# Kernel optimization log

Measured on AMD Instinct MI355X. Metric: run time of the kernel, lower is better.

The kernel has to match this reference:

```python
import jax, jax.numpy as jnp
import numpy as np

IN_FEATURES = 4096
OUT_FEATURES = 11008
N_TOKENS = 8192


def setup_inputs() -> dict:
    key = jax.random.key(0)
    kx, kw, kb = jax.random.split(key, 3)
    x = jax.random.normal(kx, (N_TOKENS, IN_FEATURES), dtype=jnp.float32)
    # nn.Linear weight: [out_features, in_features]
    bound = 1.0 / np.sqrt(IN_FEATURES)
    weight = jax.random.uniform(kw, (OUT_FEATURES, IN_FEATURES), dtype=jnp.float32,
                                minval=-bound, maxval=bound)
    bias = jax.random.uniform(kb, (OUT_FEATURES,), dtype=jnp.float32,
                              minval=-bound, maxval=bound)
    return {"x": x, "weight": weight, "bias": bias}


def reference(x, weight, bias):
    # Ternarize weights to {-1, 0, +1} then standard dense matmul + bias.
    ternary_w = jnp.sign(weight)  # [out, in]
    return jnp.matmul(x, ternary_w.T) + bias  # [n_tokens, out]
```

## Files before the change

kernel.cpp:

```cpp
#include <hip/hip_runtime.h>
#include <stdint.h>

#define M_DIM 8192
#define N_DIM 11008
#define K_DIM 4096

#define BM 256
#define BN 256
#define BK 64
#define NT (K_DIM / BK)
#define GRID_M (M_DIM / BM)
#define GRID_N (N_DIM / BN)
#define NWG (GRID_M * GRID_N)

#define BUF (BM * BK)
#define NRING 4

typedef int i32x4 __attribute__((ext_vector_type(4)));

__device__ __forceinline__ void gload16(const int8_t* src, int8_t* dst) {
    __builtin_amdgcn_global_load_lds(
        (const __attribute__((address_space(1))) uint32_t*)src,
        (__attribute__((address_space(3))) uint32_t*)dst, 16, 0, 0);
}


__global__ __launch_bounds__(256) void prepass_kernel(
    const float* __restrict__ x, int8_t* __restrict__ xq, float* __restrict__ sinv,
    const float* __restrict__ w, int8_t* __restrict__ wq, long long n16)
{
    if (blockIdx.x < 2048) {
        const int wave = blockIdx.x * 4 + (threadIdx.x >> 6);
        const int lane = threadIdx.x & 63;
        const float* row = x + (size_t)wave * K_DIM;

        float4 v[16];
        float mx = 0.0f;
        #pragma unroll
        for (int j = 0; j < 16; ++j) {
            v[j] = *(const float4*)(row + (j * 64 + lane) * 4);
            mx = fmaxf(mx, fmaxf(fmaxf(fabsf(v[j].x), fabsf(v[j].y)),
                                 fmaxf(fabsf(v[j].z), fabsf(v[j].w))));
        }
        #pragma unroll
        for (int off = 32; off > 0; off >>= 1)
            mx = fmaxf(mx, __shfl_xor(mx, off));
        if (mx < 1e-30f) mx = 1e-30f;
        const float s = 127.0f / mx;

        int8_t* orow = xq + (size_t)wave * K_DIM;
        #pragma unroll
        for (int j = 0; j < 16; ++j) {
            int a = (int)__builtin_rintf(v[j].x * s);
            int b = (int)__builtin_rintf(v[j].y * s);
            int c = (int)__builtin_rintf(v[j].z * s);
            int d = (int)__builtin_rintf(v[j].w * s);
            uint32_t p = (uint32_t)(a & 0xFF) | ((uint32_t)(b & 0xFF) << 8) |
                         ((uint32_t)(c & 0xFF) << 16) | ((uint32_t)(d & 0xFF) << 24);
            *(uint32_t*)(orow + (j * 64 + lane) * 4) = p;
        }
        if (lane == 0) sinv[wave] = mx / 127.0f;
    } else {
        long long i = (long long)(blockIdx.x - 2048) * blockDim.x + threadIdx.x;
        const long long stride = 2048LL * blockDim.x;
        for (; i < n16; i += stride) {
            const float* src = w + i * 16;
            uint32_t pk[4];
            #pragma unroll
            for (int q = 0; q < 4; ++q) {
                float4 f = *(const float4*)(src + q * 4);
                int a = (f.x > 0.f) ? 1 : ((f.x < 0.f) ? -1 : 0);
                int b = (f.y > 0.f) ? 1 : ((f.y < 0.f) ? -1 : 0);
                int c = (f.z > 0.f) ? 1 : ((f.z < 0.f) ? -1 : 0);
                int d = (f.w > 0.f) ? 1 : ((f.w < 0.f) ? -1 : 0);
                pk[q] = (uint32_t)(a & 0xFF) | ((uint32_t)(b & 0xFF) << 8) |
                        ((uint32_t)(c & 0xFF) << 16) | ((uint32_t)(d & 0xFF) << 24);
            }
            *(i32x4*)(wq + i * 16) = (i32x4){(int)pk[0], (int)pk[1], (int)pk[2], (int)pk[3]};
        }
    }
}


__global__ __launch_bounds__(1024, 4) void ternary_gemm_i8(
    const int8_t* __restrict__ A, const int8_t* __restrict__ B,
    const float* __restrict__ bias, const float* __restrict__ sinv,
    float* __restrict__ out)
{
    extern __shared__ int8_t lds[];
    int8_t* As = lds;
    int8_t* Bs = lds + NRING * BUF;

    const int tid  = threadIdx.x;
    const int lane = tid & 63;
    const int wid  = tid >> 6;
    const int wr   = wid >> 2;
    const int wc   = wid & 3;
    const int l15  = lane & 15;
    const int l4   = lane >> 4;

    const int bid = blockIdx.x;
    const int swz = (bid & 7) * (NWG / 8) + (bid >> 3);
    const int bm  = swz / GRID_N;
    const int bn  = swz % GRID_N;
    const long brow = (long)bm * BM;
    const long bcol = (long)bn * BN;

    const int rowt = tid >> 2;
    const int ssrc = (tid & 3) ^ ((tid >> 3) & 3);
    const int8_t* pA = A + (size_t)(brow + rowt) * K_DIM + ssrc * 16;
    const int8_t* pB = B + (size_t)(bcol + rowt) * K_DIM + ssrc * 16;

    auto stageAB = [&](int t, int bslot) {
        gload16(pA + (size_t)t * BK, As + bslot * BUF + tid * 16);
        gload16(pB + (size_t)t * BK, Bs + bslot * BUF + tid * 16);
    };

    const int slot = l4 ^ ((l15 >> 1) & 3);
    const int aOff = (wr * 64 + l15) * 64 + slot * 16;
    const int bOff = (wc * 64 + l15) * 64 + slot * 16;

    i32x4 acc[4][4];
    #pragma unroll
    for (int m = 0; m < 4; ++m)
        #pragma unroll
        for (int n = 0; n < 4; ++n) acc[m][n] = (i32x4){0, 0, 0, 0};

    stageAB(0, 0); stageAB(1, 1); stageAB(2, 2);
    asm volatile("s_waitcnt vmcnt(4)" ::: "memory");
    __builtin_amdgcn_s_barrier();
    __builtin_amdgcn_sched_barrier(0);

    for (int t = 0; t < NT; ++t) {
        const int b = t & 3;

        i32x4 ar[4], br[4];
        #pragma unroll
        for (int n = 0; n < 4; ++n)
            br[n] = *(const i32x4*)(Bs + b * BUF + n * 1024 + bOff);
        #pragma unroll
        for (int m = 0; m < 4; ++m)
            ar[m] = *(const i32x4*)(As + b * BUF + m * 1024 + aOff);

        if (t + 3 < NT) stageAB(t + 3, (t + 3) & 3);

        __builtin_amdgcn_s_setprio(1);
        #pragma unroll
        for (int m = 0; m < 4; ++m)
            #pragma unroll
            for (int n = 0; n < 4; ++n)
                acc[m][n] = __builtin_amdgcn_mfma_i32_16x16x64_i8(ar[m], br[n], acc[m][n], 0, 0, 0);
        __builtin_amdgcn_s_setprio(0);
        __builtin_amdgcn_sched_barrier(0);

        if (t <= NT - 4)      { asm volatile("s_waitcnt vmcnt(4)" ::: "memory"); }
        else if (t == NT - 3) { asm volatile("s_waitcnt vmcnt(2)" ::: "memory"); }
        else                  { asm volatile("s_waitcnt vmcnt(0)" ::: "memory"); }
        __builtin_amdgcn_s_barrier();
        __builtin_amdgcn_sched_barrier(0);
    }

    int   cols[4];
    float bv[4];
    #pragma unroll
    for (int n = 0; n < 4; ++n) {
        cols[n] = (int)bcol + wc * 64 + n * 16 + l15;
        bv[n] = bias[cols[n]];
    }
    #pragma unroll
    for (int m = 0; m < 4; ++m) {
        const size_t row0 = (size_t)brow + wr * 64 + m * 16 + l4 * 4;
        float s0 = sinv[row0], s1 = sinv[row0 + 1], s2 = sinv[row0 + 2], s3 = sinv[row0 + 3];
        #pragma unroll
        for (int n = 0; n < 4; ++n) {
            out[(row0 + 0) * N_DIM + cols[n]] = (float)acc[m][n][0] * s0 + bv[n];
            out[(row0 + 1) * N_DIM + cols[n]] = (float)acc[m][n][1] * s1 + bv[n];
            out[(row0 + 2) * N_DIM + cols[n]] = (float)acc[m][n][2] * s2 + bv[n];
            out[(row0 + 3) * N_DIM + cols[n]] = (float)acc[m][n][3] * s3 + bv[n];
        }
    }
}


__global__ void naive_kernel(const float* __restrict__ x, const float* __restrict__ w,
                             const float* __restrict__ bias, float* __restrict__ out) {
    long long o = (long long)blockIdx.x * blockDim.x + threadIdx.x;
    if (o >= (long long)M_DIM * N_DIM) return;
    int row = (int)(o / N_DIM), col = (int)(o % N_DIM);
    float s = 0.0f;
    const float* xr = x + (size_t)row * K_DIM;
    const float* wr = w + (size_t)col * K_DIM;
    for (int k = 0; k < K_DIM; ++k) {
        float wv = wr[k];
        s += (wv > 0.0f) ? xr[k] : ((wv < 0.0f) ? -xr[k] : 0.0f);
    }
    out[o] = s + bias[col];
}


extern "C" void kernel_launch(void* const* d_in, const int* in_sizes, int n_in,
                              void* d_out, int out_size, void* d_ws, size_t ws_size,
                              hipStream_t stream) {
    const float* x    = (const float*)d_in[0];
    const float* w    = (const float*)d_in[1];
    const float* bias = (const float*)d_in[2];
    float* out        = (float*)d_out;

    const size_t xq_bytes = (size_t)M_DIM * K_DIM;
    const size_t wq_bytes = (size_t)N_DIM * K_DIM;
    const size_t si_bytes = (size_t)M_DIM * sizeof(float);

    if (ws_size >= xq_bytes + wq_bytes + si_bytes) {
        int8_t* xq   = (int8_t*)d_ws;
        int8_t* wq   = (int8_t*)((char*)d_ws + xq_bytes);
        float*  sinv = (float*)((char*)d_ws + xq_bytes + wq_bytes);

        const long long n16 = ((long long)N_DIM * K_DIM) / 16;
        prepass_kernel<<<4096, 256, 0, stream>>>(x, xq, sinv, w, wq, n16);

        const int lds_bytes = NRING * 2 * BUF;
        hipFuncSetAttribute(reinterpret_cast<const void*>(ternary_gemm_i8),
                            hipFuncAttributeMaxDynamicSharedMemorySize, lds_bytes);
        ternary_gemm_i8<<<NWG, 1024, lds_bytes, stream>>>(xq, wq, bias, sinv, out);
    } else {
        const long long total = (long long)M_DIM * N_DIM;
        naive_kernel<<<(int)((total + 255) / 256), 256, 0, stream>>>(x, w, bias, out);
    }
}
```

Baseline: 462.0 us.

## Pre-swizzle ternary weights into MFMA fragment layout and load B directly to registers

The weight prepass now writes the int8 ternary weights in a layout that matches each wave's MFMA B-fragment order, so the GEMM loads B fragments straight from global memory into registers instead of staging them through LDS. This halves LDS usage and LDS traffic per tile, and the block ordering changes to iterate M fastest within the swizzle. The tradeoff is that B loads are no longer shared across the four waves in a row via LDS, so each B byte is fetched from global/L2 by four waves, and those direct loads sit on the critical path with no prefetch distance.

```diff
diff --git a/kernel.cpp b/kernel.cpp
--- a/kernel.cpp
+++ b/kernel.cpp
@@ -13,7 +13,7 @@
 #define GRID_N (N_DIM / BN)
 #define NWG (GRID_M * GRID_N)
 
-#define BUF (BM * BK)
+#define BUFA 16384
 #define NRING 4
 
 typedef int i32x4 __attribute__((ext_vector_type(4)));
@@ -27,7 +27,7 @@
 
 __global__ __launch_bounds__(256) void prepass_kernel(
     const float* __restrict__ x, int8_t* __restrict__ xq, float* __restrict__ sinv,
-    const float* __restrict__ w, int8_t* __restrict__ wq, long long n16)
+    const float* __restrict__ w, int8_t* __restrict__ wq)
 {
     if (blockIdx.x < 2048) {
         const int wave = blockIdx.x * 4 + (threadIdx.x >> 6);
@@ -61,10 +61,19 @@
         }
         if (lane == 0) sinv[wave] = mx / 127.0f;
     } else {
-        long long i = (long long)(blockIdx.x - 2048) * blockDim.x + threadIdx.x;
+        const long long total = 44032LL * 64;
+        long long gi = (long long)(blockIdx.x - 2048) * blockDim.x + threadIdx.x;
         const long long stride = 2048LL * blockDim.x;
-        for (; i < n16; i += stride) {
-            const float* src = w + i * 16;
+        for (; gi < total; gi += stride) {
+            const int lane  = (int)(gi & 63);
+            const long long chunk = gi >> 6;
+            const int t  = (int)(chunk & 63);
+            const int n  = (int)((chunk >> 6) & 3);
+            const int wc = (int)((chunk >> 8) & 3);
+            const int bn = (int)(chunk >> 10);
+            const int col = bn * 256 + wc * 64 + n * 16 + (lane & 15);
+            const int kb  = t * 64 + (lane >> 4) * 16;
+            const float* src = w + (size_t)col * K_DIM + kb;
             uint32_t pk[4];
             #pragma unroll
             for (int q = 0; q < 4; ++q) {
@@ -76,20 +85,20 @@
                 pk[q] = (uint32_t)(a & 0xFF) | ((uint32_t)(b & 0xFF) << 8) |
                         ((uint32_t)(c & 0xFF) << 16) | ((uint32_t)(d & 0xFF) << 24);
             }
-            *(i32x4*)(wq + i * 16) = (i32x4){(int)pk[0], (int)pk[1], (int)pk[2], (int)pk[3]};
+            *(i32x4*)(wq + chunk * 1024 + lane * 16) =
+                (i32x4){(int)pk[0], (int)pk[1], (int)pk[2], (int)pk[3]};
         }
     }
 }
 
 
 __global__ __launch_bounds__(1024, 4) void ternary_gemm_i8(
-    const int8_t* __restrict__ A, const int8_t* __restrict__ B,
+    const int8_t* __restrict__ A, const int8_t* __restrict__ Bq,
     const float* __restrict__ bias, const float* __restrict__ sinv,
     float* __restrict__ out)
 {
     extern __shared__ int8_t lds[];
     int8_t* As = lds;
-    int8_t* Bs = lds + NRING * BUF;
 
     const int tid  = threadIdx.x;
     const int lane = tid & 63;
@@ -101,24 +110,26 @@
 
     const int bid = blockIdx.x;
     const int swz = (bid & 7) * (NWG / 8) + (bid >> 3);
-    const int bm  = swz / GRID_N;
-    const int bn  = swz % GRID_N;
+    const int bm  = swz % GRID_M;
+    const int bn  = swz / GRID_M;
     const long brow = (long)bm * BM;
     const long bcol = (long)bn * BN;
 
     const int rowt = tid >> 2;
     const int ssrc = (tid & 3) ^ ((tid >> 3) & 3);
     const int8_t* pA = A + (size_t)(brow + rowt) * K_DIM + ssrc * 16;
-    const int8_t* pB = B + (size_t)(bcol + rowt) * K_DIM + ssrc * 16;
-
-    auto stageAB = [&](int t, int bslot) {
-        gload16(pA + (size_t)t * BK, As + bslot * BUF + tid * 16);
-        gload16(pB + (size_t)t * BK, Bs + bslot * BUF + tid * 16);
+
+    auto stageA = [&](int t, int bslot) {
+        gload16(pA + (size_t)t * BK, As + bslot * BUFA + tid * 16);
     };
 
     const int slot = l4 ^ ((l15 >> 1) & 3);
     const int aOff = (wr * 64 + l15) * 64 + slot * 16;
-    const int bOff = (wc * 64 + l15) * 64 + slot * 16;
+
+    const int8_t* pBn[4];
+    #pragma unroll
+    for (int n = 0; n < 4; ++n)
+        pBn[n] = Bq + ((((size_t)bn * 4 + wc) * 4 + n) * 64) * 1024 + (size_t)lane * 16;
 
     i32x4 acc[4][4];
     #pragma unroll
@@ -126,23 +137,25 @@
         #pragma unroll
         for (int n = 0; n < 4; ++n) acc[m][n] = (i32x4){0, 0, 0, 0};
 
-    stageAB(0, 0); stageAB(1, 1); stageAB(2, 2);
-    asm volatile("s_waitcnt vmcnt(4)" ::: "memory");
+    stageA(0, 0); stageA(1, 1); stageA(2, 2);
+    asm volatile("s_waitcnt vmcnt(2)" ::: "memory");
     __builtin_amdgcn_s_barrier();
     __builtin_amdgcn_sched_barrier(0);
 
     for (int t = 0; t < NT; ++t) {
         const int b = t & 3;
 
-        i32x4 ar[4], br[4];
+        i32x4 br[4];
         #pragma unroll
         for (int n = 0; n < 4; ++n)
-            br[n] = *(const i32x4*)(Bs + b * BUF + n * 1024 + bOff);
+            br[n] = *(const i32x4*)(pBn[n] + (size_t)t * 1024);
+
+        i32x4 ar[4];
         #pragma unroll
         for (int m = 0; m < 4; ++m)
-            ar[m] = *(const i32x4*)(As + b * BUF + m * 1024 + aOff);
-
-        if (t + 3 < NT) stageAB(t + 3, (t + 3) & 3);
+            ar[m] = *(const i32x4*)(As + b * BUFA + m * 1024 + aOff);
+
+        if (t + 3 < NT) stageA(t + 3, (t + 3) & 3);
 
         __builtin_amdgcn_s_setprio(1);
         #pragma unroll
@@ -153,8 +166,8 @@
         __builtin_amdgcn_s_setprio(0);
         __builtin_amdgcn_sched_barrier(0);
 
-        if (t <= NT - 4)      { asm volatile("s_waitcnt vmcnt(4)" ::: "memory"); }
-        else if (t == NT - 3) { asm volatile("s_waitcnt vmcnt(2)" ::: "memory"); }
+        if (t <= NT - 4)      { asm volatile("s_waitcnt vmcnt(2)" ::: "memory"); }
+        else if (t == NT - 3) { asm volatile("s_waitcnt vmcnt(1)" ::: "memory"); }
         else                  { asm volatile("s_waitcnt vmcnt(0)" ::: "memory"); }
         __builtin_amdgcn_s_barrier();
         __builtin_amdgcn_sched_barrier(0);
@@ -207,7 +220,7 @@
     float* out        = (float*)d_out;
 
     const size_t xq_bytes = (size_t)M_DIM * K_DIM;
-    const size_t wq_bytes = (size_t)N_DIM * K_DIM;
+    const size_t wq_bytes = 44032ULL * 1024;
     const size_t si_bytes = (size_t)M_DIM * sizeof(float);
 
     if (ws_size >= xq_bytes + wq_bytes + si_bytes) {
@@ -215,10 +228,9 @@
         int8_t* wq   = (int8_t*)((char*)d_ws + xq_bytes);
         float*  sinv = (float*)((char*)d_ws + xq_bytes + wq_bytes);
 
-        const long long n16 = ((long long)N_DIM * K_DIM) / 16;
-        prepass_kernel<<<4096, 256, 0, stream>>>(x, xq, sinv, w, wq, n16);
-
-        const int lds_bytes = NRING * 2 * BUF;
+        prepass_kernel<<<4096, 256, 0, stream>>>(x, xq, sinv, w, wq);
+
+        const int lds_bytes = NRING * BUFA;
         hipFuncSetAttribute(reinterpret_cast<const void*>(ternary_gemm_i8),
                             hipFuncAttributeMaxDynamicSharedMemorySize, lds_bytes);
         ternary_gemm_i8<<<NWG, 1024, lds_bytes, stream>>>(xq, wq, bias, sinv, out);
```

Measured after the change: 705.8 us. 1.53x slower.
